# Kernel optimization log

Hardware: AMD Instinct MI355X
Metric: run time of the kernel (lower is better)

The kernel has to match this reference:

```python
import jax, jax.numpy as jnp
import numpy as np

B, S, D, H = 2, 1024, 1024, 16
DH = D // H


def setup_inputs() -> dict:
    key = jax.random.key(0)
    k1, k2, k3 = jax.random.split(key, 3)
    x = jax.random.normal(k1, (B, S, D), dtype=jnp.float32)
    # nn.Linear weight layout: [out_features, in_features]; scaled for stable softmax logits
    W_qkv = jax.random.normal(k2, (3 * D, D), dtype=jnp.float32) * 0.02
    W_out = jax.random.normal(k3, (D, D), dtype=jnp.float32) * 0.02
    return {"x": x, "W_qkv": W_qkv, "W_out": W_out}


def reference(x, W_qkv, W_out):
    Bx, Sx, Dx = x.shape
    # fused QKV projection: [B,S,3D]
    qkv = jnp.einsum('bsd,ed->bse', x, W_qkv)
    qkv = qkv.reshape(Bx, Sx, 3, H, DH)
    q, k, v = jnp.moveaxis(qkv, 2, 0).transpose(0, 1, 3, 2, 4)
    scale = 1.0 / jnp.sqrt(jnp.asarray(DH, dtype=x.dtype))
    scores = jnp.einsum('bhqd,bhkd->bhqk', q, k) * scale  # [B,H,S,S]
    attn = jax.nn.softmax(scores, axis=-1)
    out = jnp.einsum('bhqk,bhkd->bhqd', attn, v)  # [B,H,S,DH]
    out = out.transpose(0, 2, 1, 3).reshape(Bx, Sx, Dx)  # [B,S,D]
    return jnp.einsum('bsd,ed->bse', out, W_out)
```

## Files before the change

kernel.cpp:

```cpp
#include <hip/hip_runtime.h>

#define B_  2
#define S_  1024
#define D_  1024
#define H_  16
#define DH_ 64

typedef __attribute__((ext_vector_type(8))) short bf16x8;
typedef __attribute__((ext_vector_type(4))) float f32x4;

__device__ __forceinline__ unsigned short f2bf(float f) {
  unsigned int u = __float_as_uint(f);
  u += 0x7fff + ((u >> 16) & 1);
  return (unsigned short)(u >> 16);
}

__device__ __forceinline__ unsigned int pack2bf(float a, float b) {
  return (unsigned int)f2bf(a) | ((unsigned int)f2bf(b) << 16);
}

__device__ __forceinline__ void gload_lds16(const void* g, void* l) {
  __builtin_amdgcn_global_load_lds(
      (const __attribute__((address_space(1))) unsigned int*)g,
      (__attribute__((address_space(3))) unsigned int*)l, 16, 0, 0);
}

__global__ __launch_bounds__(256)
void cvt_kernel(const float4* __restrict__ x, const float4* __restrict__ wq,
                const float4* __restrict__ wo, unsigned short* __restrict__ xb,
                unsigned short* __restrict__ wqb, unsigned short* __restrict__ wob) {
  constexpr int n1 = (B_*S_*D_) / 4;
  constexpr int n2 = (3*D_*D_) / 4;
  constexpr int n3 = (D_*D_) / 4;
  for (int i = blockIdx.x*blockDim.x + threadIdx.x; i < n1+n2+n3;
       i += gridDim.x*blockDim.x) {
    const float4* src; unsigned short* dst; int off;
    if (i < n1)          { src = x;  dst = xb;  off = i; }
    else if (i < n1+n2)  { src = wq; dst = wqb; off = i - n1; }
    else                 { src = wo; dst = wob; off = i - n1 - n2; }
    float4 v = src[off];
    ushort4 r;
    r.x = f2bf(v.x); r.y = f2bf(v.y); r.z = f2bf(v.z); r.w = f2bf(v.w);
    *(ushort4*)&dst[off*4] = r;
  }
}

template<int BM, int M, int N, int K, int EPI>
__global__ __launch_bounds__(256)
void gemm_bt(const unsigned short* __restrict__ A, const unsigned short* __restrict__ Bw,
             float* __restrict__ C, unsigned short* __restrict__ Qb,
             unsigned short* __restrict__ Kb, unsigned short* __restrict__ Vtb) {
  constexpr int NBN = N / 128;
  constexpr int MT  = BM / 32;
  constexpr int AH  = BM / 64;
  constexpr int NSTEP = K / 32;
  __shared__ unsigned short As[3][BM*32];
  __shared__ unsigned short Bs[3][128*32];
  const int tid = threadIdx.x;
  const int bid = blockIdx.x;
  const int mb = bid / NBN, nb = bid % NBN;
  const int wid = tid >> 6, lane = tid & 63;
  const int wr = wid >> 1, wc = wid & 1;
  const int lg = lane >> 4, lr = lane & 15;

  f32x4 acc[MT][4] = {};

  const int mrow = mb*BM, nrow = nb*128;
  const int srow = tid >> 2;
  const int scol = (tid & 3) * 8;

  auto STAGE = [&](int t) {
    const int k0 = t*32, b = t % 3;
    #pragma unroll
    for (int h = 0; h < AH; ++h)
      gload_lds16(A  + (size_t)(mrow + h*64 + srow)*K + k0 + scol, &As[b][(h*256 + tid)*8]);
    #pragma unroll
    for (int h = 0; h < 2; ++h)
      gload_lds16(Bw + (size_t)(nrow + h*64 + srow)*K + k0 + scol, &Bs[b][(h*256 + tid)*8]);
  };

  STAGE(0);
  STAGE(1);
  for (int t = 0; t < NSTEP; ++t) {
    if (t < NSTEP-1) {
      if constexpr (AH == 1) asm volatile("s_waitcnt vmcnt(3)" ::: "memory");
      else                   asm volatile("s_waitcnt vmcnt(4)" ::: "memory");
    } else {
      asm volatile("s_waitcnt vmcnt(0)" ::: "memory");
    }
    __builtin_amdgcn_s_barrier();
    __builtin_amdgcn_sched_barrier(0);
    if (t + 2 < NSTEP) STAGE(t+2);
    const int b = t % 3;
    bf16x8 af[MT], bfr[4];
    #pragma unroll
    for (int m = 0; m < MT; ++m)
      af[m]  = *(const bf16x8*)&As[b][(wr*(BM/2) + m*16 + lr)*32 + lg*8];
    #pragma unroll
    for (int n = 0; n < 4; ++n)
      bfr[n] = *(const bf16x8*)&Bs[b][(wc*64 + n*16 + lr)*32 + lg*8];
    #pragma unroll
    for (int m = 0; m < MT; ++m)
      #pragma unroll
      for (int n = 0; n < 4; ++n)
        acc[m][n] = __builtin_amdgcn_mfma_f32_16x16x32_bf16(af[m], bfr[n], acc[m][n], 0, 0, 0);
  }

  #pragma unroll
  for (int mt = 0; mt < MT; ++mt) {
    const int m0 = mrow + wr*(BM/2) + mt*16 + lg*4;
    #pragma unroll
    for (int nt = 0; nt < 4; ++nt) {
      const int n = nrow + wc*64 + nt*16 + lr;
      f32x4 v = acc[mt][nt];
      if constexpr (EPI == 0) {
        #pragma unroll
        for (int i = 0; i < 4; ++i) C[(size_t)(m0 + i)*N + n] = v[i];
      } else {
        const int t3 = n >> 10, rem = n & 1023;
        const int hh = rem >> 6, dh = rem & 63;
        const int b = m0 >> 10, s0 = m0 & 1023;
        if (t3 == 2) {
          ushort4 pk;
          pk.x = f2bf(v[0]); pk.y = f2bf(v[1]); pk.z = f2bf(v[2]); pk.w = f2bf(v[3]);
          *(ushort4*)&Vtb[(size_t)((b*H_ + hh)*DH_ + dh)*S_ + s0] = pk;
        } else {
          unsigned short* dst = (t3 == 0) ? Qb : Kb;
          #pragma unroll
          for (int i = 0; i < 4; ++i)
            dst[(size_t)((b*H_ + hh)*S_ + s0 + i)*DH_ + dh] = f2bf(v[i]);
        }
      }
    }
  }
}

__global__ __launch_bounds__(256, 2)
void attn_kernel(const unsigned short* __restrict__ Qb, const unsigned short* __restrict__ Kb,
                 const unsigned short* __restrict__ Vtb, unsigned short* __restrict__ AOb) {
  __shared__ unsigned short Ks[3][64*64];
  __shared__ unsigned short Vs[3][64*64];
  __shared__ unsigned short Pl[4][16*72];
  const int bid = blockIdx.x;
  const int xcd = bid & 7, rr = bid >> 3;
  const int qt = rr & 15;
  const int bh = (rr >> 4) * 8 + xcd;
  const int tid = threadIdx.x, wid = tid >> 6, lane = tid & 63;
  const int lg = lane >> 4, lr = lane & 15;
  const unsigned short* Q  = Qb  + (size_t)bh*S_*DH_;
  const unsigned short* Kp = Kb  + (size_t)bh*S_*DH_;
  const unsigned short* Vt = Vtb + (size_t)bh*DH_*S_;
  const int q0 = qt*64 + wid*16;

  bf16x8 qf0 = *(const bf16x8*)&Q[(size_t)(q0 + lr)*DH_ + lg*8];
  bf16x8 qf1 = *(const bf16x8*)&Q[(size_t)(q0 + lr)*DH_ + 32 + lg*8];

  const int sr = tid >> 3;
  const int g0 = (tid & 7) ^ (sr & 7);

  float mrun = -1e30f, lrun = 0.f;
  f32x4 o[4] = {};
  const int rsw = lr & 7;

  auto STAGE = [&](int t) {
    const int j = t * 64, b = t % 3;
    gload_lds16(Kp + (size_t)(j + sr)*DH_      + g0*8, &Ks[b][tid*8]);
    gload_lds16(Kp + (size_t)(j + sr + 32)*DH_ + g0*8, &Ks[b][(256+tid)*8]);
    gload_lds16(Vt + (size_t)sr*S_      + j + g0*8,    &Vs[b][tid*8]);
    gload_lds16(Vt + (size_t)(sr+32)*S_ + j + g0*8,    &Vs[b][(256+tid)*8]);
  };

  STAGE(0);
  STAGE(1);
  for (int t = 0; t < 16; ++t) {
    if (t < 15) asm volatile("s_waitcnt vmcnt(4)" ::: "memory");
    else        asm volatile("s_waitcnt vmcnt(0)" ::: "memory");
    __builtin_amdgcn_s_barrier();
    __builtin_amdgcn_sched_barrier(0);
    if (t + 2 < 16) STAGE(t+2);
    const int buf = t % 3;
    f32x4 sv[4];
    __builtin_amdgcn_s_setprio(1);
    #pragma unroll
    for (int f = 0; f < 4; ++f) {
      bf16x8 ka = *(const bf16x8*)&Ks[buf][(16*f + lr)*64 + ((lg     ^ rsw)*8)];
      bf16x8 kb = *(const bf16x8*)&Ks[buf][(16*f + lr)*64 + (((lg+4) ^ rsw)*8)];
      f32x4 z = {};
      z     = __builtin_amdgcn_mfma_f32_16x16x32_bf16(ka, qf0, z, 0, 0, 0);
      sv[f] = __builtin_amdgcn_mfma_f32_16x16x32_bf16(kb, qf1, z, 0, 0, 0);
    }
    __builtin_amdgcn_s_setprio(0);
    float s[16];
    #pragma unroll
    for (int f = 0; f < 4; ++f)
      #pragma unroll
      for (int i = 0; i < 4; ++i) s[4*f + i] = sv[f][i] * 0.125f;
    float t8[8];
    #pragma unroll
    for (int k = 0; k < 8; ++k) t8[k] = fmaxf(s[k], s[k+8]);
    float t4a = fmaxf(t8[0], t8[4]), t4b = fmaxf(t8[1], t8[5]);
    float t4c = fmaxf(t8[2], t8[6]), t4d = fmaxf(t8[3], t8[7]);
    float pmax = fmaxf(fmaxf(t4a, t4b), fmaxf(t4c, t4d));
    pmax = fmaxf(pmax, __shfl_xor(pmax, 16));
    pmax = fmaxf(pmax, __shfl_xor(pmax, 32));
    float mnew = fmaxf(mrun, pmax);
    float cr = __expf(mrun - mnew);
    float p[16];
    #pragma unroll
    for (int k = 0; k < 16; ++k) p[k] = __expf(s[k] - mnew);
    float u8[8];
    #pragma unroll
    for (int k = 0; k < 8; ++k) u8[k] = p[k] + p[k+8];
    float u4a = u8[0]+u8[4], u4b = u8[1]+u8[5], u4c = u8[2]+u8[6], u4d = u8[3]+u8[7];
    float rs = (u4a + u4b) + (u4c + u4d);
    rs += __shfl_xor(rs, 16);
    rs += __shfl_xor(rs, 32);
    lrun = lrun*cr + rs;
    mrun = mnew;
    #pragma unroll
    for (int f = 0; f < 4; ++f) {
      uint2 w;
      w.x = pack2bf(p[4*f],   p[4*f+1]);
      w.y = pack2bf(p[4*f+2], p[4*f+3]);
      *(uint2*)&Pl[wid][lr*72 + f*16 + lg*4] = w;
    }
    #pragma unroll
    for (int dt = 0; dt < 4; ++dt) {
      o[dt][0] *= cr; o[dt][1] *= cr; o[dt][2] *= cr; o[dt][3] *= cr;
    }
    asm volatile("s_waitcnt lgkmcnt(0)" ::: "memory");
    __builtin_amdgcn_sched_barrier(0);
    __builtin_amdgcn_s_setprio(1);
    #pragma unroll
    for (int c = 0; c < 2; ++c) {
      bf16x8 pf = *(const bf16x8*)&Pl[wid][lr*72 + c*32 + lg*8];
      #pragma unroll
      for (int dt = 0; dt < 4; ++dt) {
        bf16x8 vfr = *(const bf16x8*)&Vs[buf][(dt*16 + lr)*64 + (((c*4 + lg) ^ rsw)*8)];
        o[dt] = __builtin_amdgcn_mfma_f32_16x16x32_bf16(vfr, pf, o[dt], 0, 0, 0);
      }
    }
    __builtin_amdgcn_s_setprio(0);
  }

  const float inv = 1.0f / lrun;
  const int b = bh >> 4, hh = bh & 15;
  #pragma unroll
  for (int dt = 0; dt < 4; ++dt) {
    ushort4 pk;
    pk.x = f2bf(o[dt][0]*inv); pk.y = f2bf(o[dt][1]*inv);
    pk.z = f2bf(o[dt][2]*inv); pk.w = f2bf(o[dt][3]*inv);
    *(ushort4*)&AOb[(size_t)(b*S_ + q0 + lr)*D_ + hh*DH_ + dt*16 + lg*4] = pk;
  }
}

extern "C" void kernel_launch(void* const* d_in, const int* in_sizes, int n_in,
                              void* d_out, int out_size, void* d_ws, size_t ws_size,
                              hipStream_t stream) {
  const float* x  = (const float*)d_in[0];
  const float* wq = (const float*)d_in[1];
  const float* wo = (const float*)d_in[2];
  float* out = (float*)d_out;

  unsigned short* w = (unsigned short*)d_ws;
  unsigned short* xb  = w;
  unsigned short* wqb = xb  + 2097152;
  unsigned short* wob = wqb + 3145728;
  unsigned short* qb  = wob + 1048576;
  unsigned short* kb  = qb  + 2097152;
  unsigned short* vtb = kb  + 2097152;
  unsigned short* aob = vtb + 2097152;

  cvt_kernel<<<dim3(1024), dim3(256), 0, stream>>>(
      (const float4*)x, (const float4*)wq, (const float4*)wo, xb, wqb, wob);

  gemm_bt<64, 2048, 3072, 1024, 1><<<dim3(32*24), dim3(256), 0, stream>>>(
      xb, wqb, nullptr, qb, kb, vtb);

  attn_kernel<<<dim3(512), dim3(256), 0, stream>>>(qb, kb, vtb, aob);

  gemm_bt<64, 2048, 1024, 1024, 0><<<dim3(32*8), dim3(256), 0, stream>>>(
      aob, wob, out, nullptr, nullptr, nullptr);
}
```

Baseline: 140.3 us.

## Replace block-shared GEMM with per-wave private tiles and split-K output projection

Rewrites the GEMM so each wave in a 128-thread block owns a private 64x64 output tile with its own triple-buffered LDS staging. This removes the block-wide barrier in the K loop. The output projection splits K across the two waves and reduces the partial sums through LDS, giving twice as many blocks on the smaller GEMM. Blocks are remapped across XCDs by a swizzle. In exchange there is no LDS sharing of A/B tiles between waves, which raises global and L2 traffic per FLOP.

```diff
diff --git a/kernel.cpp b/kernel.cpp
--- a/kernel.cpp
+++ b/kernel.cpp
@@ -45,91 +45,111 @@
   }
 }
 
-template<int BM, int M, int N, int K, int EPI>
-__global__ __launch_bounds__(256)
-void gemm_bt(const unsigned short* __restrict__ A, const unsigned short* __restrict__ Bw,
+template<int NTM, int NTN, int K, int EPI, int KHALF>
+__global__ __launch_bounds__(128)
+void gemm_wv(const unsigned short* __restrict__ A, const unsigned short* __restrict__ Bw,
              float* __restrict__ C, unsigned short* __restrict__ Qb,
              unsigned short* __restrict__ Kb, unsigned short* __restrict__ Vtb) {
-  constexpr int NBN = N / 128;
-  constexpr int MT  = BM / 32;
-  constexpr int AH  = BM / 64;
-  constexpr int NSTEP = K / 32;
-  __shared__ unsigned short As[3][BM*32];
-  __shared__ unsigned short Bs[3][128*32];
-  const int tid = threadIdx.x;
-  const int bid = blockIdx.x;
-  const int mb = bid / NBN, nb = bid % NBN;
-  const int wid = tid >> 6, lane = tid & 63;
-  const int wr = wid >> 1, wc = wid & 1;
+  constexpr int KW    = KHALF ? K/2 : K;
+  constexpr int NSTEP = KW / 32;
+  __shared__ unsigned short L[2][3][2][64*32];
+  __shared__ float Ored[KHALF ? 64*64 : 1];
+  const int tid = threadIdx.x, wid = tid >> 6, lane = tid & 63;
   const int lg = lane >> 4, lr = lane & 15;
 
-  f32x4 acc[MT][4] = {};
-
-  const int mrow = mb*BM, nrow = nb*128;
-  const int srow = tid >> 2;
-  const int scol = (tid & 3) * 8;
+  const int nblk = gridDim.x;
+  const int sb = (blockIdx.x & 7) * (nblk >> 3) + (blockIdx.x >> 3);
+  int mw, nw, kbase;
+  if constexpr (KHALF) {
+    mw = sb % NTM; nw = sb / NTM; kbase = wid * KW;
+  } else {
+    const int wt = sb*2 + wid;
+    mw = wt % NTM; nw = wt / NTM; kbase = 0;
+  }
+  const int m0 = mw*64, n0 = nw*64;
+  const unsigned short* Ap = A  + kbase;
+  const unsigned short* Bp = Bw + kbase;
+
+  f32x4 acc[4][4] = {};
 
   auto STAGE = [&](int t) {
     const int k0 = t*32, b = t % 3;
-    #pragma unroll
-    for (int h = 0; h < AH; ++h)
-      gload_lds16(A  + (size_t)(mrow + h*64 + srow)*K + k0 + scol, &As[b][(h*256 + tid)*8]);
-    #pragma unroll
-    for (int h = 0; h < 2; ++h)
-      gload_lds16(Bw + (size_t)(nrow + h*64 + srow)*K + k0 + scol, &Bs[b][(h*256 + tid)*8]);
+    unsigned short* LA = &L[wid][b][0][0];
+    unsigned short* LB = &L[wid][b][1][0];
+    const int row = (lane >> 2), lc = lane & 3;
+    #pragma unroll
+    for (int g = 0; g < 4; ++g) {
+      gload_lds16(Ap + (size_t)(m0 + g*16 + row)*K + k0 + lc*8, &LA[(g*64 + lane)*8]);
+      gload_lds16(Bp + (size_t)(n0 + g*16 + row)*K + k0 + lc*8, &LB[(g*64 + lane)*8]);
+    }
   };
 
   STAGE(0);
   STAGE(1);
   for (int t = 0; t < NSTEP; ++t) {
-    if (t < NSTEP-1) {
-      if constexpr (AH == 1) asm volatile("s_waitcnt vmcnt(3)" ::: "memory");
-      else                   asm volatile("s_waitcnt vmcnt(4)" ::: "memory");
-    } else {
-      asm volatile("s_waitcnt vmcnt(0)" ::: "memory");
-    }
-    __builtin_amdgcn_s_barrier();
+    if (t < NSTEP-1) asm volatile("s_waitcnt vmcnt(8)" ::: "memory");
+    else             asm volatile("s_waitcnt vmcnt(0)" ::: "memory");
     __builtin_amdgcn_sched_barrier(0);
+    const int b = t % 3;
+    const unsigned short* LA = &L[wid][b][0][0];
+    const unsigned short* LB = &L[wid][b][1][0];
+    bf16x8 af[4], bf[4];
+    #pragma unroll
+    for (int m = 0; m < 4; ++m) af[m] = *(const bf16x8*)&LA[(m*16 + lr)*32 + lg*8];
+    #pragma unroll
+    for (int n = 0; n < 4; ++n) bf[n] = *(const bf16x8*)&LB[(n*16 + lr)*32 + lg*8];
     if (t + 2 < NSTEP) STAGE(t+2);
-    const int b = t % 3;
-    bf16x8 af[MT], bfr[4];
-    #pragma unroll
-    for (int m = 0; m < MT; ++m)
-      af[m]  = *(const bf16x8*)&As[b][(wr*(BM/2) + m*16 + lr)*32 + lg*8];
-    #pragma unroll
-    for (int n = 0; n < 4; ++n)
-      bfr[n] = *(const bf16x8*)&Bs[b][(wc*64 + n*16 + lr)*32 + lg*8];
-    #pragma unroll
-    for (int m = 0; m < MT; ++m)
+    #pragma unroll
+    for (int m = 0; m < 4; ++m)
       #pragma unroll
       for (int n = 0; n < 4; ++n)
-        acc[m][n] = __builtin_amdgcn_mfma_f32_16x16x32_bf16(af[m], bfr[n], acc[m][n], 0, 0, 0);
-  }
-
-  #pragma unroll
-  for (int mt = 0; mt < MT; ++mt) {
-    const int m0 = mrow + wr*(BM/2) + mt*16 + lg*4;
-    #pragma unroll
-    for (int nt = 0; nt < 4; ++nt) {
-      const int n = nrow + wc*64 + nt*16 + lr;
-      f32x4 v = acc[mt][nt];
-      if constexpr (EPI == 0) {
+        acc[m][n] = __builtin_amdgcn_mfma_f32_16x16x32_bf16(af[m], bf[n], acc[m][n], 0, 0, 0);
+  }
+
+  if constexpr (KHALF) {
+    if (wid == 1) {
+      #pragma unroll
+      for (int mt = 0; mt < 4; ++mt)
         #pragma unroll
-        for (int i = 0; i < 4; ++i) C[(size_t)(m0 + i)*N + n] = v[i];
-      } else {
-        const int t3 = n >> 10, rem = n & 1023;
-        const int hh = rem >> 6, dh = rem & 63;
-        const int b = m0 >> 10, s0 = m0 & 1023;
-        if (t3 == 2) {
-          ushort4 pk;
-          pk.x = f2bf(v[0]); pk.y = f2bf(v[1]); pk.z = f2bf(v[2]); pk.w = f2bf(v[3]);
-          *(ushort4*)&Vtb[(size_t)((b*H_ + hh)*DH_ + dh)*S_ + s0] = pk;
-        } else {
-          unsigned short* dst = (t3 == 0) ? Qb : Kb;
+        for (int nt = 0; nt < 4; ++nt)
           #pragma unroll
           for (int i = 0; i < 4; ++i)
-            dst[(size_t)((b*H_ + hh)*S_ + s0 + i)*DH_ + dh] = f2bf(v[i]);
-        }
+            Ored[(mt*16 + lg*4 + i)*64 + nt*16 + lr] = acc[mt][nt][i];
+    }
+    __syncthreads();
+    if (wid == 0) {
+      #pragma unroll
+      for (int mt = 0; mt < 4; ++mt)
+        #pragma unroll
+        for (int nt = 0; nt < 4; ++nt)
+          #pragma unroll
+          for (int i = 0; i < 4; ++i) {
+            const int m = m0 + mt*16 + lg*4 + i, n = n0 + nt*16 + lr;
+            C[(size_t)m*(NTN*64) + n] = acc[mt][nt][i] + Ored[(mt*16 + lg*4 + i)*64 + nt*16 + lr];
+          }
+    }
+    return;
+  }
+
+  #pragma unroll
+  for (int mt = 0; mt < 4; ++mt) {
+    const int mm0 = m0 + mt*16 + lg*4;
+    #pragma unroll
+    for (int nt = 0; nt < 4; ++nt) {
+      const int n = n0 + nt*16 + lr;
+      f32x4 v = acc[mt][nt];
+      const int t3 = n >> 10, rem = n & 1023;
+      const int hh = rem >> 6, dh = rem & 63;
+      const int b = mm0 >> 10, s0 = mm0 & 1023;
+      if (t3 == 2) {
+        ushort4 pk;
+        pk.x = f2bf(v[0]); pk.y = f2bf(v[1]); pk.z = f2bf(v[2]); pk.w = f2bf(v[3]);
+        *(ushort4*)&Vtb[(size_t)((b*H_ + hh)*DH_ + dh)*S_ + s0] = pk;
+      } else {
+        unsigned short* dst = (t3 == 0) ? Qb : Kb;
+        #pragma unroll
+        for (int i = 0; i < 4; ++i)
+          dst[(size_t)((b*H_ + hh)*S_ + s0 + i)*DH_ + dh] = f2bf(v[i]);
       }
     }
   }
@@ -274,11 +294,11 @@
   cvt_kernel<<<dim3(1024), dim3(256), 0, stream>>>(
       (const float4*)x, (const float4*)wq, (const float4*)wo, xb, wqb, wob);
 
-  gemm_bt<64, 2048, 3072, 1024, 1><<<dim3(32*24), dim3(256), 0, stream>>>(
+  gemm_wv<32, 48, 1024, 1, 0><<<dim3(768), dim3(128), 0, stream>>>(
       xb, wqb, nullptr, qb, kb, vtb);
 
   attn_kernel<<<dim3(512), dim3(256), 0, stream>>>(qb, kb, vtb, aob);
 
-  gemm_bt<64, 2048, 1024, 1024, 0><<<dim3(32*8), dim3(256), 0, stream>>>(
+  gemm_wv<32, 16, 1024, 0, 1><<<dim3(512), dim3(128), 0, stream>>>(
       aob, wob, out, nullptr, nullptr, nullptr);
 }
```

Result: faster. 135.5 us (-3.4%).
